# Kernel tuning notes

Measured on AMD Instinct MI355X. Metric: run time of the kernel, lower is better.

Reference implementation:

```python
import jax, jax.numpy as jnp
import numpy as np

EPS = 1e-5

def conv2d(x, w, b, pad):
    # x: [B,C,H,W], w: [O,I,kh,kw] (OIHW), b: [O]
    y = jax.lax.conv_general_dilated(x, w, (1, 1), [(pad, pad), (pad, pad)],
                                     dimension_numbers=('NCHW', 'OIHW', 'NCHW'))
    return y + b[None, :, None, None]

def bn(x, g, b, m, v):
    # eval-mode BatchNorm2d
    scale = (g / jnp.sqrt(v + EPS))[None, :, None, None]
    return (x - m[None, :, None, None]) * scale + b[None, :, None, None]


def setup_inputs() -> dict:
    key = jax.random.key(0)
    ks = jax.random.split(key, 16)
    B, C, H, W = 2, 64, 64, 64
    Cq = C // 8
    f = lambda k, shp, s=0.05: jax.random.normal(k, shp, dtype=jnp.float32) * s
    return {
        'x': jax.random.normal(ks[0], (B, C, H, W), dtype=jnp.float32),
        'sW': f(ks[1], (C, C, 3, 3)), 'sb': f(ks[2], (C,)),
        's_g': jnp.ones((C,), jnp.float32), 's_b': jnp.zeros((C,), jnp.float32),
        's_m': jnp.zeros((C,), jnp.float32), 's_v': jnp.ones((C,), jnp.float32),
        'cW': f(ks[3], (C, C, 3, 3)), 'cb': f(ks[4], (C,)),
        'c_g': jnp.ones((C,), jnp.float32), 'c_b': jnp.zeros((C,), jnp.float32),
        'c_m': jnp.zeros((C,), jnp.float32), 'c_v': jnp.ones((C,), jnp.float32),
        'qW': f(ks[5], (Cq, C, 1, 1)), 'qb': f(ks[6], (Cq,)),
        'kW': f(ks[7], (Cq, C, 1, 1)), 'kb': f(ks[8], (Cq,)),
        'vW': f(ks[9], (C, C, 1, 1)), 'vb': f(ks[10], (C,)),
        'oW': f(ks[11], (C, C, 1, 1)), 'ob': f(ks[12], (C,)),
        's_gamma': jnp.array([0.5], jnp.float32),
        'c_gamma': jnp.array([0.5], jnp.float32),
    }


def reference(x, sW, sb, s_g, s_b, s_m, s_v, cW, cb, c_g, c_b, c_m, c_v,
              qW, qb, kW, kb, vW, vb, oW, ob, s_gamma, c_gamma):
    # ---- spatial attention branch ----
    s_x = jax.nn.relu(bn(conv2d(x, sW, sb, 1), s_g, s_b, s_m, s_v))  # [B,C,H,W]
    B, C, H, W = s_x.shape
    HW = H * W
    q = conv2d(x, qW, qb, 0).reshape(B, -1, HW)  # [B, C/8, HW]
    k = conv2d(x, kW, kb, 0).reshape(B, -1, HW)  # [B, C/8, HW]
    v = conv2d(x, vW, vb, 0).reshape(B, C, HW)   # [B, C,   HW]
    # aff[b,i,j] = q_i . k_j ; softmax over j (unscaled, per original)
    A = jax.nn.softmax(jnp.einsum('bdi,bdj->bij', q, k), axis=-1)  # [B,HW,HW]
    sa = jnp.einsum('bcj,bij->bci', v, A).reshape(B, C, H, W)
    sa_map = s_gamma[0] * sa + s_x
    # ---- channel attention branch ----
    c_x = jax.nn.relu(bn(conv2d(x, cW, cb, 1), c_g, c_b, c_m, c_v))  # [B,C,H,W]
    fmap = c_x.reshape(B, C, HW)
    Ac = jnp.einsum('bin,bjn->bij', fmap, fmap)  # [B,C,C]
    Ac = jax.nn.softmax(jnp.max(Ac, axis=-1, keepdims=True) - Ac, axis=-1)
    ca = jnp.einsum('bij,bjn->bin', Ac, fmap).reshape(B, C, H, W)
    ca_map = c_gamma[0] * ca + c_x
    # ---- fuse + output adaptor ----
    return conv2d(sa_map + ca_map, oW, ob, 0)
```

## Files before the change

### kernel.cpp

```cpp
#include <hip/hip_runtime.h>

#define HW 4096

typedef __attribute__((ext_vector_type(8)))  short short8;
typedef __attribute__((ext_vector_type(16))) float float16;

__device__ __forceinline__ unsigned short f2bf(float f) {
    unsigned u = __float_as_uint(f);
    u += 0x7fffu + ((u >> 16) & 1u);
    return (unsigned short)(u >> 16);
}

__global__ __launch_bounds__(256) void k_wprep(
    const float* __restrict__ sW, const float* __restrict__ cW,
    const float* __restrict__ sb, const float* __restrict__ cb,
    const float* __restrict__ s_g, const float* __restrict__ s_b,
    const float* __restrict__ s_m, const float* __restrict__ s_v,
    const float* __restrict__ c_g, const float* __restrict__ c_b,
    const float* __restrict__ c_m, const float* __restrict__ c_v,
    unsigned short* __restrict__ Wa, float* __restrict__ scsh)
{
    int bx = blockIdx.x;
    int which = bx / 9, khw = bx % 9;
    const float* W = which ? cW : sW;
    int t = threadIdx.x;
#pragma unroll
    for (int i = 0; i < 16; i++) {
        int idx = t + 256 * i;
        int oc = idx >> 6, ic = idx & 63;
        float v = W[(size_t)(oc * 64 + ic) * 9 + khw];
        Wa[((size_t)(which * 9 + khw) * 64 + oc) * 64 + ic] = f2bf(v);
    }
    if (bx == 0 && t < 128) {
        int wh = t >> 6, oc = t & 63;
        const float* g  = wh ? c_g : s_g;
        const float* bb = wh ? c_b : s_b;
        const float* m  = wh ? c_m : s_m;
        const float* vv = wh ? c_v : s_v;
        const float* cbias = wh ? cb : sb;
        float scale = g[oc] * rsqrtf(vv[oc] + 1e-5f);
        scsh[wh * 128 + oc]      = scale;
        scsh[wh * 128 + 64 + oc] = (cbias[oc] - m[oc]) * scale + bb[oc];
    }
}

__global__ __launch_bounds__(256) void k_conv_qkv(
    const float* __restrict__ x, const unsigned short* __restrict__ Wa,
    const float* __restrict__ scsh,
    const float* __restrict__ qW, const float* __restrict__ qb,
    const float* __restrict__ kW, const float* __restrict__ kb,
    const float* __restrict__ vW, const float* __restrict__ vb,
    float* __restrict__ sx, float* __restrict__ cx,
    unsigned short* __restrict__ qT, unsigned short* __restrict__ kT,
    unsigned short* __restrict__ vB)
{
    __shared__ unsigned short xs[3 * 8 * 66 * 8];
    int bx = blockIdx.x;
    int t = threadIdx.x;

    if (bx < 256) {
        int which = bx >> 7;
        int b     = (bx >> 6) & 1;
        int row   = bx & 63;

        const float* xb = x + (size_t)(b * 64) * HW;
#pragma unroll
        for (int it = 0; it < 24; it++) {
            int idx = t + 256 * it;
            int lr  = idx >> 11;
            int rem = idx & 2047;
            int icp = rem >> 6;
            int col = rem & 63;
            int ir  = row - 1 + lr;
            unsigned pack = 0;
            if (ir >= 0 && ir < 64) {
                float v0 = xb[(size_t)(icp * 2)     * HW + ir * 64 + col];
                float v1 = xb[(size_t)(icp * 2 + 1) * HW + ir * 64 + col];
                pack = (unsigned)f2bf(v0) | ((unsigned)f2bf(v1) << 16);
            }
            int icg = icp >> 2, io = icp & 3;
            *(unsigned*)&xs[(((lr * 8 + icg) * 66 + col + 1) * 8) + io * 2] = pack;
        }
        if (t < 192) {
            int pair = t & 3;
            int colsel = (t >> 2) & 1;
            int rg = t >> 3;
            *(unsigned*)&xs[((rg * 66 + colsel * 65) * 8) + pair * 2] = 0u;
        }
        __syncthreads();

        int lane = t & 63, w = t >> 6;
        int l31 = lane & 31, half = lane >> 5;
        int colh = w & 1;
        int m0   = (w >> 1) * 32;
        int c    = colh * 32 + l31;

        float16 acc;
#pragma unroll
        for (int i = 0; i < 16; i++) acc[i] = 0.f;

        const unsigned short* Wbase =
            Wa + ((size_t)which * 9) * 4096 + (size_t)(m0 + l31) * 64 + half * 8;

#pragma unroll
        for (int khw = 0; khw < 9; khw++) {
            const int kh = khw / 3, kw = khw % 3;
#pragma unroll
            for (int icq = 0; icq < 4; icq++) {
                short8 af = *(const short8*)(Wbase + (size_t)khw * 4096 + icq * 16);
                const unsigned short* bp =
                    &xs[((kh * 8 + icq * 2 + half) * 66 + kw) * 8];
                short8 bf = *(const short8*)(bp + (size_t)c * 8);
                acc = __builtin_amdgcn_mfma_f32_32x32x16_bf16(af, bf, acc, 0, 0, 0);
            }
        }

        float* out = (which ? cx : sx) + (size_t)(b * 64) * HW;
        const float* sc = scsh + which * 128;
        int hwbase = row * 64 + c;
#pragma unroll
        for (int r = 0; r < 16; r++) {
            int oc = m0 + (r & 3) + 8 * (r >> 2) + 4 * half;
            float s  = sc[oc];
            float sh = sc[64 + oc];
            out[(size_t)oc * HW + hwbase] = fmaxf(acc[r] * s + sh, 0.f);
        }
    } else {
        int qbx = bx - 256;
        int b = qbx / 80, rem = qbx % 80;
        int chunk = rem / 5, g = rem % 5;
        int hw = chunk * 256 + t;
        const float* xb = x + (size_t)(b * 64) * HW + hw;

        float acc[16];
#pragma unroll
        for (int u = 0; u < 16; u++) acc[u] = 0.f;

        if (g == 0) {
            for (int ic = 0; ic < 64; ic++) {
                float xv = xb[ic * HW];
#pragma unroll
                for (int u = 0; u < 8; u++) acc[u]     += qW[u * 64 + ic] * xv;
#pragma unroll
                for (int u = 0; u < 8; u++) acc[8 + u] += kW[u * 64 + ic] * xv;
            }
            short8 qv, kv;
#pragma unroll
            for (int u = 0; u < 8; u++) qv[u] = (short)f2bf(acc[u] + qb[u]);
#pragma unroll
            for (int u = 0; u < 8; u++) kv[u] = (short)f2bf(acc[8 + u] + kb[u]);
            *(short8*)(qT + ((size_t)(b * HW) + hw) * 8) = qv;
            *(short8*)(kT + ((size_t)(b * HW) + hw) * 8) = kv;
        } else {
            int c0 = (g - 1) * 16;
            for (int ic = 0; ic < 64; ic++) {
                float xv = xb[ic * HW];
#pragma unroll
                for (int u = 0; u < 16; u++) acc[u] += vW[(c0 + u) * 64 + ic] * xv;
            }
            int m  = hw & 15;
            int sg = (m & 3) | ((m & 4) << 1) | ((m & 8) >> 1);
            size_t base = ((size_t)(b * 256) + (hw >> 4)) * 1024 + sg;
#pragma unroll
            for (int u = 0; u < 16; u++)
                vB[base + (size_t)(c0 + u) * 16] = f2bf(acc[u] + vb[c0 + u]);
        }
    }
}

union SmemKB {
    struct { float o_sh[4][64][33]; float den_sh[4][32]; } a;
    float slab[32][68];
};

__global__ __launch_bounds__(256) void k_attn_gram(
    const unsigned short* __restrict__ qT, const unsigned short* __restrict__ kT,
    const unsigned short* __restrict__ vB, const float* __restrict__ cx,
    float* __restrict__ Opart, float* __restrict__ denp,
    float* __restrict__ Gpart)
{
    __shared__ SmemKB sm;
    int bx = blockIdx.x;
    int t = threadIdx.x;

    if (bx < 512) {
        int lane = t & 63, w = t >> 6;
        int half = lane >> 5, l31 = lane & 31;
        int b  = bx >> 8;
        int itile = (bx >> 1) & 127;
        int jh = bx & 1;
        int i0 = itile * 32;

        short8 qf;
        if (half == 0) {
            qf = *(const short8*)(qT + ((size_t)(b * HW) + i0 + l31) * 8);
        } else {
#pragma unroll
            for (int i = 0; i < 8; i++) qf[i] = 0;
        }

        float16 o0, o1;
#pragma unroll
        for (int i = 0; i < 16; i++) { o0[i] = 0.f; o1[i] = 0.f; }
        float denr = 0.f;

        const unsigned short* kTb = kT + (size_t)(b * HW) * 8;
        const unsigned short* vBb = vB + (size_t)b * (256 * 1024);

        for (int tile = 0; tile < 16; tile++) {
            int j0 = jh * 2048 + w * 512 + tile * 32;
            int g0 = j0 >> 4;

            short8 kf;
            if (half == 0) {
                kf = *(const short8*)(kTb + (size_t)(j0 + l31) * 8);
            } else {
#pragma unroll
                for (int i = 0; i < 8; i++) kf[i] = 0;
            }

            float16 z;
#pragma unroll
            for (int i = 0; i < 16; i++) z[i] = 0.f;
            float16 s = __builtin_amdgcn_mfma_f32_32x32x16_bf16(kf, qf, z, 0, 0, 0);

            float p[16];
#pragma unroll
            for (int r = 0; r < 16; r++) {
                p[r] = __expf(s[r]);
                denr += p[r];
            }
            short8 pa0, pa1;
#pragma unroll
            for (int r = 0; r < 8; r++) {
                pa0[r] = (short)f2bf(p[r]);
                pa1[r] = (short)f2bf(p[8 + r]);
            }

            const unsigned short* vg0 = vBb + (size_t)g0 * 1024 + half * 8;
            short8 v00 = *(const short8*)(vg0 + (size_t)l31 * 16);
            short8 v01 = *(const short8*)(vg0 + (size_t)(32 + l31) * 16);
            short8 v10 = *(const short8*)(vg0 + 1024 + (size_t)l31 * 16);
            short8 v11 = *(const short8*)(vg0 + 1024 + (size_t)(32 + l31) * 16);

            o0 = __builtin_amdgcn_mfma_f32_32x32x16_bf16(pa0, v00, o0, 0, 0, 0);
            o1 = __builtin_amdgcn_mfma_f32_32x32x16_bf16(pa0, v01, o1, 0, 0, 0);
            o0 = __builtin_amdgcn_mfma_f32_32x32x16_bf16(pa1, v10, o0, 0, 0, 0);
            o1 = __builtin_amdgcn_mfma_f32_32x32x16_bf16(pa1, v11, o1, 0, 0, 0);
        }

        float dfull = denr + __shfl_xor(denr, 32);
        if (half == 0) sm.a.den_sh[w][l31] = dfull;
#pragma unroll
        for (int r = 0; r < 16; r++) {
            int il = (r & 3) + 8 * (r >> 2) + 4 * half;
            sm.a.o_sh[w][l31][il]      = o0[r];
            sm.a.o_sh[w][32 + l31][il] = o1[r];
        }
        __syncthreads();

        int i  = t & 31;
        int cg = t >> 5;
        if (cg == 0)
            denp[jh * 8192 + b * 4096 + i0 + i] =
                sm.a.den_sh[0][i] + sm.a.den_sh[1][i] +
                sm.a.den_sh[2][i] + sm.a.den_sh[3][i];
#pragma unroll
        for (int u = 0; u < 8; u++) {
            int c = cg * 8 + u;
            float sv = sm.a.o_sh[0][c][i] + sm.a.o_sh[1][c][i]
                     + sm.a.o_sh[2][c][i] + sm.a.o_sh[3][c][i];
            Opart[((size_t)(jh * 2 + b) * 64 + c) * HW + i0 + i] = sv;
        }
    } else {
        int gbx = bx - 512;
        int b = gbx >> 7, slice = gbx & 127;
        int hw0 = slice * 32;

#pragma unroll
        for (int it = 0; it < 2; it++) {
            int idx = t + 256 * it;
            int hw = idx & 31, c0 = (idx >> 5) * 4;
            float4 vv;
            vv.x = cx[(size_t)(b * 64 + c0 + 0) * HW + hw0 + hw];
            vv.y = cx[(size_t)(b * 64 + c0 + 1) * HW + hw0 + hw];
            vv.z = cx[(size_t)(b * 64 + c0 + 2) * HW + hw0 + hw];
            vv.w = cx[(size_t)(b * 64 + c0 + 3) * HW + hw0 + hw];
            *(float4*)&sm.slab[hw][c0] = vv;
        }
        __syncthreads();

        int i0 = (t & 15) * 4, j0 = (t >> 4) * 4;
        float acc[4][4] = {};
#pragma unroll 8
        for (int hw = 0; hw < 32; hw++) {
            float4 ai = *(const float4*)&sm.slab[hw][i0];
            float4 aj = *(const float4*)&sm.slab[hw][j0];
            acc[0][0] += ai.x * aj.x; acc[0][1] += ai.x * aj.y;
            acc[0][2] += ai.x * aj.z; acc[0][3] += ai.x * aj.w;
            acc[1][0] += ai.y * aj.x; acc[1][1] += ai.y * aj.y;
            acc[1][2] += ai.y * aj.z; acc[1][3] += ai.y * aj.w;
            acc[2][0] += ai.z * aj.x; acc[2][1] += ai.z * aj.y;
            acc[2][2] += ai.z * aj.z; acc[2][3] += ai.z * aj.w;
            acc[3][0] += ai.w * aj.x; acc[3][1] += ai.w * aj.y;
            acc[3][2] += ai.w * aj.z; acc[3][3] += ai.w * aj.w;
        }

        float* Gb = Gpart + ((size_t)(b * 128 + slice) * 64) * 64;
#pragma unroll
        for (int ii = 0; ii < 4; ii++)
            *(float4*)&Gb[(size_t)(i0 + ii) * 64 + j0] =
                make_float4(acc[ii][0], acc[ii][1], acc[ii][2], acc[ii][3]);
    }
}

__global__ __launch_bounds__(64) void k_csoft(
    const float* __restrict__ Gpart, float* __restrict__ AcsT)
{
    int row = blockIdx.x;
    int b = row >> 6, i = row & 63;
    int j = threadIdx.x;

    const float* Gp = Gpart + ((size_t)(b * 128) * 64 + i) * 64 + j;
    float a = 0.f;
#pragma unroll 4
    for (int sl = 0; sl < 128; sl++)
        a += Gp[(size_t)sl * 4096];

    float mn = a;
    mn = fminf(mn, __shfl_xor(mn, 1));
    mn = fminf(mn, __shfl_xor(mn, 2));
    mn = fminf(mn, __shfl_xor(mn, 4));
    mn = fminf(mn, __shfl_xor(mn, 8));
    mn = fminf(mn, __shfl_xor(mn, 16));
    mn = fminf(mn, __shfl_xor(mn, 32));
    float p = __expf(mn - a);
    float s = p;
    s += __shfl_xor(s, 1);
    s += __shfl_xor(s, 2);
    s += __shfl_xor(s, 4);
    s += __shfl_xor(s, 8);
    s += __shfl_xor(s, 16);
    s += __shfl_xor(s, 32);
    AcsT[(size_t)b * 4096 + j * 64 + i] = p / s;
}

__global__ __launch_bounds__(256) void k_fuse_out(
    const float* __restrict__ Opart, const float* __restrict__ denp,
    const float* __restrict__ sx,    const float* __restrict__ cx,
    const float* __restrict__ AcsT,
    const float* __restrict__ oW,    const float* __restrict__ ob,
    const float* __restrict__ s_gamma, const float* __restrict__ c_gamma,
    float* __restrict__ out)
{
    __shared__ float A_sh[64][68];
    __shared__ float cxs[64][33];
    __shared__ float f_sh[64][33];
    __shared__ float oWT[64][68];

    int bx = blockIdx.x;
    int b = bx >> 7, chunk = bx & 127;
    int px0 = chunk * 32;
    int t = threadIdx.x;
    float sgam = s_gamma[0], cgam = c_gamma[0];

#pragma unroll
    for (int k = 0; k < 16; k++) {
        int idx = t + 256 * k;
        int j = idx >> 6, i = idx & 63;
        A_sh[j][i] = AcsT[(size_t)b * 4096 + idx];
        oWT[j][i]  = oW[(size_t)i * 64 + j];
    }
#pragma unroll
    for (int k = 0; k < 8; k++) {
        int idx = t + 256 * k;
        int c = idx >> 5, px = idx & 31;
        size_t o = (size_t)(b * 64 + c) * HW + px0 + px;
        float cv = cx[o];
        cxs[c][px] = cv;
        float d = denp[b * 4096 + px0 + px] + denp[8192 + b * 4096 + px0 + px];
        float O = Opart[((size_t)(b)*64 + c) * HW + px0 + px]
                + Opart[((size_t)(2 + b) * 64 + c) * HW + px0 + px];
        f_sh[c][px] = sgam * (O / d) + sx[o] + cv;
    }
    __syncthreads();

    {
        int px = t & 31, cg = t >> 5;
        int c0 = cg * 8;
        float ca[8] = {};
        for (int j = 0; j < 64; j++) {
            float xv = cxs[j][px];
            float4 a0 = *(const float4*)&A_sh[j][c0];
            float4 a1 = *(const float4*)&A_sh[j][c0 + 4];
            ca[0] += a0.x * xv; ca[1] += a0.y * xv;
            ca[2] += a0.z * xv; ca[3] += a0.w * xv;
            ca[4] += a1.x * xv; ca[5] += a1.y * xv;
            ca[6] += a1.z * xv; ca[7] += a1.w * xv;
        }
#pragma unroll
        for (int u = 0; u < 8; u++)
            f_sh[c0 + u][px] += cgam * ca[u];
    }
    __syncthreads();

    {
        int px = t & 31, og = t >> 5;
        int o0 = og * 8;
        float acc[8] = {};
        for (int c = 0; c < 64; c++) {
            float fv = f_sh[c][px];
            float4 a0 = *(const float4*)&oWT[c][o0];
            float4 a1 = *(const float4*)&oWT[c][o0 + 4];
            acc[0] += a0.x * fv; acc[1] += a0.y * fv;
            acc[2] += a0.z * fv; acc[3] += a0.w * fv;
            acc[4] += a1.x * fv; acc[5] += a1.y * fv;
            acc[6] += a1.z * fv; acc[7] += a1.w * fv;
        }
#pragma unroll
        for (int u = 0; u < 8; u++) {
            int o = o0 + u;
            out[(size_t)(b * 64 + o) * HW + px0 + px] = acc[u] + ob[o];
        }
    }
}

extern "C" void kernel_launch(void* const* d_in, const int* in_sizes, int n_in,
                              void* d_out, int out_size, void* d_ws, size_t ws_size,
                              hipStream_t stream)
{
    const float* x    = (const float*)d_in[0];
    const float* sW   = (const float*)d_in[1];
    const float* sb   = (const float*)d_in[2];
    const float* s_g  = (const float*)d_in[3];
    const float* s_b  = (const float*)d_in[4];
    const float* s_m  = (const float*)d_in[5];
    const float* s_v  = (const float*)d_in[6];
    const float* cW   = (const float*)d_in[7];
    const float* cb   = (const float*)d_in[8];
    const float* c_g  = (const float*)d_in[9];
    const float* c_b  = (const float*)d_in[10];
    const float* c_m  = (const float*)d_in[11];
    const float* c_v  = (const float*)d_in[12];
    const float* qW   = (const float*)d_in[13];
    const float* qb   = (const float*)d_in[14];
    const float* kW   = (const float*)d_in[15];
    const float* kb   = (const float*)d_in[16];
    const float* vW   = (const float*)d_in[17];
    const float* vb   = (const float*)d_in[18];
    const float* oW   = (const float*)d_in[19];
    const float* ob   = (const float*)d_in[20];
    const float* s_gamma = (const float*)d_in[21];
    const float* c_gamma = (const float*)d_in[22];

    float* ws    = (float*)d_ws;
    float* sx    = ws;
    float* cx    = ws + 524288;
    float* Opart = ws + 1048576;
    float* denp  = ws + 2097152;
    float* AcsT  = ws + 2113536;
    float* Gpart = ws + 2121728;
    float* scsh  = ws + 3170304;
    unsigned short* us = (unsigned short*)(ws + 3170560);
    unsigned short* qT = us;
    unsigned short* kT = us + 65536;
    unsigned short* vB = us + 131072;
    unsigned short* Wa = us + 655360;

    k_wprep<<<18, 256, 0, stream>>>(sW, cW, sb, cb, s_g, s_b, s_m, s_v,
                                    c_g, c_b, c_m, c_v, Wa, scsh);
    k_conv_qkv<<<416, 256, 0, stream>>>(x, Wa, scsh, qW, qb, kW, kb, vW, vb,
                                        sx, cx, qT, kT, vB);
    k_attn_gram<<<768, 256, 0, stream>>>(qT, kT, vB, cx, Opart, denp, Gpart);
    k_csoft<<<128, 64, 0, stream>>>(Gpart, AcsT);
    k_fuse_out<<<256, 256, 0, stream>>>(Opart, denp, sx, cx, AcsT,
                                        oW, ob, s_gamma, c_gamma, (float*)d_out);
}
```

Baseline: 170.9 us.

## Fuse all stages into one persistent kernel with grid-wide barriers

Merges the five separate launches (weight prep, conv/QKV, attention+Gram, channel softmax, fuse/output) into a single 512-block kernel separated by atomic-counter grid barriers. It also reshapes work along the way: fewer, larger Gram slices, and a single-block channel softmax per batch. The oW transpose moves into the prep stage, and the output stage uses 16-pixel chunks across all 512 blocks. The goal is to remove inter-kernel launch gaps and tail idle time. In exchange it relies on all 512 blocks being co-resident and on a barrier reset trick that assumes the counter cell holds a 0xAA fill pattern before each call.

```diff
diff --git a/kernel.cpp b/kernel.cpp
--- a/kernel.cpp
+++ b/kernel.cpp
@@ -1,6 +1,7 @@
 #include <hip/hip_runtime.h>
 
 #define HW 4096
+#define NBLK 512
 
 typedef __attribute__((ext_vector_type(8)))  short short8;
 typedef __attribute__((ext_vector_type(16))) float float16;
@@ -11,59 +12,87 @@
     return (unsigned short)(u >> 16);
 }
 
-__global__ __launch_bounds__(256) void k_wprep(
-    const float* __restrict__ sW, const float* __restrict__ cW,
-    const float* __restrict__ sb, const float* __restrict__ cb,
-    const float* __restrict__ s_g, const float* __restrict__ s_b,
-    const float* __restrict__ s_m, const float* __restrict__ s_v,
-    const float* __restrict__ c_g, const float* __restrict__ c_b,
-    const float* __restrict__ c_m, const float* __restrict__ c_v,
-    unsigned short* __restrict__ Wa, float* __restrict__ scsh)
+struct Params {
+    const float *x;
+    const float *sW, *sb, *s_g, *s_b, *s_m, *s_v;
+    const float *cW, *cb, *c_g, *c_b, *c_m, *c_v;
+    const float *qW, *qb, *kW, *kb, *vW, *vb, *oW, *ob;
+    const float *s_gamma, *c_gamma;
+    float *out;
+    float *sx, *cx, *Opart, *denp, *ATg, *Gpart, *oWTg, *scsh;
+    unsigned *bar;
+    unsigned short *qT, *kT, *vB, *Wa;
+};
+
+union SmemAll {
+    unsigned short xs[3 * 8 * 66 * 8];
+    struct { float o_sh[4][64][33]; float den_sh[4][32]; } at;
+    float slab[64][68];
+    struct {
+        float AT[64][68];
+        union {
+            float A_raw[64][68];
+            struct { float cxs[64][17]; float f_sh[64][17];
+                     float oWT[64][68]; } f;
+        } u;
+    } d;
+};
+
+__device__ __forceinline__ void gridbar(unsigned* cell)
 {
+    __syncthreads();
+    if (threadIdx.x == 0) {
+        __threadfence();
+        atomicCAS(cell, 0xAAAAAAAAu, 0u);
+        atomicAdd(cell, 1u);
+        while (atomicAdd(cell, 0u) < NBLK) __builtin_amdgcn_s_sleep(8);
+        __threadfence();
+    }
+    __syncthreads();
+}
+
+__global__ __launch_bounds__(256, 2) void k_mega(Params p)
+{
+    __shared__ SmemAll sm;
     int bx = blockIdx.x;
-    int which = bx / 9, khw = bx % 9;
-    const float* W = which ? cW : sW;
-    int t = threadIdx.x;
-#pragma unroll
-    for (int i = 0; i < 16; i++) {
-        int idx = t + 256 * i;
-        int oc = idx >> 6, ic = idx & 63;
-        float v = W[(size_t)(oc * 64 + ic) * 9 + khw];
-        Wa[((size_t)(which * 9 + khw) * 64 + oc) * 64 + ic] = f2bf(v);
-    }
-    if (bx == 0 && t < 128) {
-        int wh = t >> 6, oc = t & 63;
-        const float* g  = wh ? c_g : s_g;
-        const float* bb = wh ? c_b : s_b;
-        const float* m  = wh ? c_m : s_m;
-        const float* vv = wh ? c_v : s_v;
-        const float* cbias = wh ? cb : sb;
-        float scale = g[oc] * rsqrtf(vv[oc] + 1e-5f);
-        scsh[wh * 128 + oc]      = scale;
-        scsh[wh * 128 + 64 + oc] = (cbias[oc] - m[oc]) * scale + bb[oc];
-    }
-}
-
-__global__ __launch_bounds__(256) void k_conv_qkv(
-    const float* __restrict__ x, const unsigned short* __restrict__ Wa,
-    const float* __restrict__ scsh,
-    const float* __restrict__ qW, const float* __restrict__ qb,
-    const float* __restrict__ kW, const float* __restrict__ kb,
-    const float* __restrict__ vW, const float* __restrict__ vb,
-    float* __restrict__ sx, float* __restrict__ cx,
-    unsigned short* __restrict__ qT, unsigned short* __restrict__ kT,
-    unsigned short* __restrict__ vB)
-{
-    __shared__ unsigned short xs[3 * 8 * 66 * 8];
-    int bx = blockIdx.x;
-    int t = threadIdx.x;
+    int t  = threadIdx.x;
+
+    if (bx < 18) {
+        int which = bx / 9, khw = bx % 9;
+        const float* W = which ? p.cW : p.sW;
+#pragma unroll
+        for (int i = 0; i < 16; i++) {
+            int idx = t + 256 * i;
+            int oc = idx >> 6, ic = idx & 63;
+            float v = W[(size_t)(oc * 64 + ic) * 9 + khw];
+            p.Wa[((size_t)(which * 9 + khw) * 64 + oc) * 64 + ic] = f2bf(v);
+        }
+        if (bx == 0 && t < 128) {
+            int wh = t >> 6, oc = t & 63;
+            const float* g  = wh ? p.c_g : p.s_g;
+            const float* bb = wh ? p.c_b : p.s_b;
+            const float* m  = wh ? p.c_m : p.s_m;
+            const float* vv = wh ? p.c_v : p.s_v;
+            const float* cbias = wh ? p.cb : p.sb;
+            float scale = g[oc] * rsqrtf(vv[oc] + 1e-5f);
+            p.scsh[wh * 128 + oc]      = scale;
+            p.scsh[wh * 128 + 64 + oc] = (cbias[oc] - m[oc]) * scale + bb[oc];
+        }
+    } else if (bx == 18) {
+#pragma unroll
+        for (int k = 0; k < 16; k++) {
+            int idx = t + 256 * k;
+            int c = idx >> 6, o = idx & 63;
+            p.oWTg[idx] = p.oW[(size_t)o * 64 + c];
+        }
+    }
+    gridbar(p.bar + 0);
 
     if (bx < 256) {
         int which = bx >> 7;
         int b     = (bx >> 6) & 1;
         int row   = bx & 63;
-
-        const float* xb = x + (size_t)(b * 64) * HW;
+        const float* xb = p.x + (size_t)(b * 64) * HW;
 #pragma unroll
         for (int it = 0; it < 24; it++) {
             int idx = t + 256 * it;
@@ -79,13 +108,13 @@
                 pack = (unsigned)f2bf(v0) | ((unsigned)f2bf(v1) << 16);
             }
             int icg = icp >> 2, io = icp & 3;
-            *(unsigned*)&xs[(((lr * 8 + icg) * 66 + col + 1) * 8) + io * 2] = pack;
+            *(unsigned*)&sm.xs[(((lr * 8 + icg) * 66 + col + 1) * 8) + io * 2] = pack;
         }
         if (t < 192) {
             int pair = t & 3;
             int colsel = (t >> 2) & 1;
             int rg = t >> 3;
-            *(unsigned*)&xs[((rg * 66 + colsel * 65) * 8) + pair * 2] = 0u;
+            *(unsigned*)&sm.xs[((rg * 66 + colsel * 65) * 8) + pair * 2] = 0u;
         }
         __syncthreads();
 
@@ -100,7 +129,7 @@
         for (int i = 0; i < 16; i++) acc[i] = 0.f;
 
         const unsigned short* Wbase =
-            Wa + ((size_t)which * 9) * 4096 + (size_t)(m0 + l31) * 64 + half * 8;
+            p.Wa + ((size_t)which * 9) * 4096 + (size_t)(m0 + l31) * 64 + half * 8;
 
 #pragma unroll
         for (int khw = 0; khw < 9; khw++) {
@@ -109,14 +138,14 @@
             for (int icq = 0; icq < 4; icq++) {
                 short8 af = *(const short8*)(Wbase + (size_t)khw * 4096 + icq * 16);
                 const unsigned short* bp =
-                    &xs[((kh * 8 + icq * 2 + half) * 66 + kw) * 8];
+                    &sm.xs[((kh * 8 + icq * 2 + half) * 66 + kw) * 8];
                 short8 bf = *(const short8*)(bp + (size_t)c * 8);
                 acc = __builtin_amdgcn_mfma_f32_32x32x16_bf16(af, bf, acc, 0, 0, 0);
             }
         }
 
-        float* out = (which ? cx : sx) + (size_t)(b * 64) * HW;
-        const float* sc = scsh + which * 128;
+        float* out = (which ? p.cx : p.sx) + (size_t)(b * 64) * HW;
+        const float* sc = p.scsh + which * 128;
         int hwbase = row * 64 + c;
 #pragma unroll
         for (int r = 0; r < 16; r++) {
@@ -125,12 +154,12 @@
             float sh = sc[64 + oc];
             out[(size_t)oc * HW + hwbase] = fmaxf(acc[r] * s + sh, 0.f);
         }
-    } else {
-        int qbx = bx - 256;
-        int b = qbx / 80, rem = qbx % 80;
+    } else if (bx < 416) {
+        int ubx = bx - 256;
+        int b = ubx / 80, rem = ubx % 80;
         int chunk = rem / 5, g = rem % 5;
         int hw = chunk * 256 + t;
-        const float* xb = x + (size_t)(b * 64) * HW + hw;
+        const float* xb = p.x + (size_t)(b * 64) * HW + hw;
 
         float acc[16];
 #pragma unroll
@@ -140,50 +169,35 @@
             for (int ic = 0; ic < 64; ic++) {
                 float xv = xb[ic * HW];
 #pragma unroll
-                for (int u = 0; u < 8; u++) acc[u]     += qW[u * 64 + ic] * xv;
-#pragma unroll
-                for (int u = 0; u < 8; u++) acc[8 + u] += kW[u * 64 + ic] * xv;
+                for (int u = 0; u < 8; u++) acc[u]     += p.qW[u * 64 + ic] * xv;
+#pragma unroll
+                for (int u = 0; u < 8; u++) acc[8 + u] += p.kW[u * 64 + ic] * xv;
             }
             short8 qv, kv;
 #pragma unroll
-            for (int u = 0; u < 8; u++) qv[u] = (short)f2bf(acc[u] + qb[u]);
-#pragma unroll
-            for (int u = 0; u < 8; u++) kv[u] = (short)f2bf(acc[8 + u] + kb[u]);
-            *(short8*)(qT + ((size_t)(b * HW) + hw) * 8) = qv;
-            *(short8*)(kT + ((size_t)(b * HW) + hw) * 8) = kv;
+            for (int u = 0; u < 8; u++) qv[u] = (short)f2bf(acc[u] + p.qb[u]);
+#pragma unroll
+            for (int u = 0; u < 8; u++) kv[u] = (short)f2bf(acc[8 + u] + p.kb[u]);
+            *(short8*)(p.qT + ((size_t)(b * HW) + hw) * 8) = qv;
+            *(short8*)(p.kT + ((size_t)(b * HW) + hw) * 8) = kv;
         } else {
             int c0 = (g - 1) * 16;
             for (int ic = 0; ic < 64; ic++) {
                 float xv = xb[ic * HW];
 #pragma unroll
-                for (int u = 0; u < 16; u++) acc[u] += vW[(c0 + u) * 64 + ic] * xv;
+                for (int u = 0; u < 16; u++) acc[u] += p.vW[(c0 + u) * 64 + ic] * xv;
             }
             int m  = hw & 15;
             int sg = (m & 3) | ((m & 4) << 1) | ((m & 8) >> 1);
             size_t base = ((size_t)(b * 256) + (hw >> 4)) * 1024 + sg;
 #pragma unroll
             for (int u = 0; u < 16; u++)
-                vB[base + (size_t)(c0 + u) * 16] = f2bf(acc[u] + vb[c0 + u]);
-        }
-    }
-}
-
-union SmemKB {
-    struct { float o_sh[4][64][33]; float den_sh[4][32]; } a;
-    float slab[32][68];
-};
-
-__global__ __launch_bounds__(256) void k_attn_gram(
-    const unsigned short* __restrict__ qT, const unsigned short* __restrict__ kT,
-    const unsigned short* __restrict__ vB, const float* __restrict__ cx,
-    float* __restrict__ Opart, float* __restrict__ denp,
-    float* __restrict__ Gpart)
-{
-    __shared__ SmemKB sm;
-    int bx = blockIdx.x;
-    int t = threadIdx.x;
-
-    if (bx < 512) {
+                p.vB[base + (size_t)(c0 + u) * 16] = f2bf(acc[u] + p.vb[c0 + u]);
+        }
+    }
+    gridbar(p.bar + 1);
+
+    {
         int lane = t & 63, w = t >> 6;
         int half = lane >> 5, l31 = lane & 31;
         int b  = bx >> 8;
@@ -193,7 +207,7 @@
 
         short8 qf;
         if (half == 0) {
-            qf = *(const short8*)(qT + ((size_t)(b * HW) + i0 + l31) * 8);
+            qf = *(const short8*)(p.qT + ((size_t)(b * HW) + i0 + l31) * 8);
         } else {
 #pragma unroll
             for (int i = 0; i < 8; i++) qf[i] = 0;
@@ -204,8 +218,8 @@
         for (int i = 0; i < 16; i++) { o0[i] = 0.f; o1[i] = 0.f; }
         float denr = 0.f;
 
-        const unsigned short* kTb = kT + (size_t)(b * HW) * 8;
-        const unsigned short* vBb = vB + (size_t)b * (256 * 1024);
+        const unsigned short* kTb = p.kT + (size_t)(b * HW) * 8;
+        const unsigned short* vBb = p.vB + (size_t)b * (256 * 1024);
 
         for (int tile = 0; tile < 16; tile++) {
             int j0 = jh * 2048 + w * 512 + tile * 32;
@@ -224,17 +238,17 @@
             for (int i = 0; i < 16; i++) z[i] = 0.f;
             float16 s = __builtin_amdgcn_mfma_f32_32x32x16_bf16(kf, qf, z, 0, 0, 0);
 
-            float p[16];
+            float pr[16];
 #pragma unroll
             for (int r = 0; r < 16; r++) {
-                p[r] = __expf(s[r]);
-                denr += p[r];
+                pr[r] = __expf(s[r]);
+                denr += pr[r];
             }
             short8 pa0, pa1;
 #pragma unroll
             for (int r = 0; r < 8; r++) {
-                pa0[r] = (short)f2bf(p[r]);
-                pa1[r] = (short)f2bf(p[8 + r]);
+                pa0[r] = (short)f2bf(pr[r]);
+                pa1[r] = (short)f2bf(pr[8 + r]);
             }
 
             const unsigned short* vg0 = vBb + (size_t)g0 * 1024 + half * 8;
@@ -250,177 +264,154 @@
         }
 
         float dfull = denr + __shfl_xor(denr, 32);
-        if (half == 0) sm.a.den_sh[w][l31] = dfull;
+        if (half == 0) sm.at.den_sh[w][l31] = dfull;
 #pragma unroll
         for (int r = 0; r < 16; r++) {
             int il = (r & 3) + 8 * (r >> 2) + 4 * half;
-            sm.a.o_sh[w][l31][il]      = o0[r];
-            sm.a.o_sh[w][32 + l31][il] = o1[r];
+            sm.at.o_sh[w][l31][il]      = o0[r];
+            sm.at.o_sh[w][32 + l31][il] = o1[r];
         }
         __syncthreads();
 
         int i  = t & 31;
         int cg = t >> 5;
         if (cg == 0)
-            denp[jh * 8192 + b * 4096 + i0 + i] =
-                sm.a.den_sh[0][i] + sm.a.den_sh[1][i] +
-                sm.a.den_sh[2][i] + sm.a.den_sh[3][i];
+            p.denp[jh * 8192 + b * 4096 + i0 + i] =
+                sm.at.den_sh[0][i] + sm.at.den_sh[1][i] +
+                sm.at.den_sh[2][i] + sm.at.den_sh[3][i];
 #pragma unroll
         for (int u = 0; u < 8; u++) {
             int c = cg * 8 + u;
-            float sv = sm.a.o_sh[0][c][i] + sm.a.o_sh[1][c][i]
-                     + sm.a.o_sh[2][c][i] + sm.a.o_sh[3][c][i];
-            Opart[((size_t)(jh * 2 + b) * 64 + c) * HW + i0 + i] = sv;
-        }
-    } else {
-        int gbx = bx - 512;
-        int b = gbx >> 7, slice = gbx & 127;
-        int hw0 = slice * 32;
-
-#pragma unroll
-        for (int it = 0; it < 2; it++) {
-            int idx = t + 256 * it;
-            int hw = idx & 31, c0 = (idx >> 5) * 4;
-            float4 vv;
-            vv.x = cx[(size_t)(b * 64 + c0 + 0) * HW + hw0 + hw];
-            vv.y = cx[(size_t)(b * 64 + c0 + 1) * HW + hw0 + hw];
-            vv.z = cx[(size_t)(b * 64 + c0 + 2) * HW + hw0 + hw];
-            vv.w = cx[(size_t)(b * 64 + c0 + 3) * HW + hw0 + hw];
-            *(float4*)&sm.slab[hw][c0] = vv;
+            float sv = sm.at.o_sh[0][c][i] + sm.at.o_sh[1][c][i]
+                     + sm.at.o_sh[2][c][i] + sm.at.o_sh[3][c][i];
+            p.Opart[((size_t)(jh * 2 + b) * 64 + c) * HW + i0 + i] = sv;
+        }
+    }
+    if (bx >= 448) {
+        int gbx = bx - 448;
+        int b = gbx >> 5, slice = gbx & 31;
+        int i0 = (t & 15) * 4, j0c = (t >> 4) * 4;
+        float acc[4][4] = {};
+#pragma unroll
+        for (int ch = 0; ch < 2; ch++) {
+            int hwb = slice * 128 + ch * 64;
+            __syncthreads();
+#pragma unroll
+            for (int it = 0; it < 16; it++) {
+                int idx = t + 256 * it;
+                int hw = idx & 63, c = idx >> 6;
+                sm.slab[hw][c] = p.cx[(size_t)(b * 64 + c) * HW + hwb + hw];
+            }
+            __syncthreads();
+#pragma unroll 8
+            for (int hw = 0; hw < 64; hw++) {
+                float4 ai = *(const float4*)&sm.slab[hw][i0];
+                float4 aj = *(const float4*)&sm.slab[hw][j0c];
+                acc[0][0] += ai.x * aj.x; acc[0][1] += ai.x * aj.y;
+                acc[0][2] += ai.x * aj.z; acc[0][3] += ai.x * aj.w;
+                acc[1][0] += ai.y * aj.x; acc[1][1] += ai.y * aj.y;
+                acc[1][2] += ai.y * aj.z; acc[1][3] += ai.y * aj.w;
+                acc[2][0] += ai.z * aj.x; acc[2][1] += ai.z * aj.y;
+                acc[2][2] += ai.z * aj.z; acc[2][3] += ai.z * aj.w;
+                acc[3][0] += ai.w * aj.x; acc[3][1] += ai.w * aj.y;
+                acc[3][2] += ai.w * aj.z; acc[3][3] += ai.w * aj.w;
+            }
+        }
+        float* Gb = p.Gpart + ((size_t)(b * 32 + slice)) * 4096;
+#pragma unroll
+        for (int ii = 0; ii < 4; ii++)
+            *(float4*)&Gb[(size_t)(i0 + ii) * 64 + j0c] =
+                make_float4(acc[ii][0], acc[ii][1], acc[ii][2], acc[ii][3]);
+    }
+    gridbar(p.bar + 2);
+
+    if (bx < 2) {
+        int b = bx;
+#pragma unroll
+        for (int k = 0; k < 16; k++) {
+            int idx = t + 256 * k;
+            float a = 0.f;
+#pragma unroll 8
+            for (int sl = 0; sl < 32; sl++)
+                a += p.Gpart[((size_t)(b * 32 + sl)) * 4096 + idx];
+            sm.d.u.A_raw[idx >> 6][idx & 63] = a;
         }
         __syncthreads();
-
-        int i0 = (t & 15) * 4, j0 = (t >> 4) * 4;
-        float acc[4][4] = {};
+        if (t < 64) {
+            int i = t;
+            float mn = sm.d.u.A_raw[i][0];
 #pragma unroll 8
-        for (int hw = 0; hw < 32; hw++) {
-            float4 ai = *(const float4*)&sm.slab[hw][i0];
-            float4 aj = *(const float4*)&sm.slab[hw][j0];
-            acc[0][0] += ai.x * aj.x; acc[0][1] += ai.x * aj.y;
-            acc[0][2] += ai.x * aj.z; acc[0][3] += ai.x * aj.w;
-            acc[1][0] += ai.y * aj.x; acc[1][1] += ai.y * aj.y;
-            acc[1][2] += ai.y * aj.z; acc[1][3] += ai.y * aj.w;
-            acc[2][0] += ai.z * aj.x; acc[2][1] += ai.z * aj.y;
-            acc[2][2] += ai.z * aj.z; acc[2][3] += ai.z * aj.w;
-            acc[3][0] += ai.w * aj.x; acc[3][1] += ai.w * aj.y;
-            acc[3][2] += ai.w * aj.z; acc[3][3] += ai.w * aj.w;
-        }
-
-        float* Gb = Gpart + ((size_t)(b * 128 + slice) * 64) * 64;
-#pragma unroll
-        for (int ii = 0; ii < 4; ii++)
-            *(float4*)&Gb[(size_t)(i0 + ii) * 64 + j0] =
-                make_float4(acc[ii][0], acc[ii][1], acc[ii][2], acc[ii][3]);
-    }
-}
-
-__global__ __launch_bounds__(64) void k_csoft(
-    const float* __restrict__ Gpart, float* __restrict__ AcsT)
-{
-    int row = blockIdx.x;
-    int b = row >> 6, i = row & 63;
-    int j = threadIdx.x;
-
-    const float* Gp = Gpart + ((size_t)(b * 128) * 64 + i) * 64 + j;
-    float a = 0.f;
-#pragma unroll 4
-    for (int sl = 0; sl < 128; sl++)
-        a += Gp[(size_t)sl * 4096];
-
-    float mn = a;
-    mn = fminf(mn, __shfl_xor(mn, 1));
-    mn = fminf(mn, __shfl_xor(mn, 2));
-    mn = fminf(mn, __shfl_xor(mn, 4));
-    mn = fminf(mn, __shfl_xor(mn, 8));
-    mn = fminf(mn, __shfl_xor(mn, 16));
-    mn = fminf(mn, __shfl_xor(mn, 32));
-    float p = __expf(mn - a);
-    float s = p;
-    s += __shfl_xor(s, 1);
-    s += __shfl_xor(s, 2);
-    s += __shfl_xor(s, 4);
-    s += __shfl_xor(s, 8);
-    s += __shfl_xor(s, 16);
-    s += __shfl_xor(s, 32);
-    AcsT[(size_t)b * 4096 + j * 64 + i] = p / s;
-}
-
-__global__ __launch_bounds__(256) void k_fuse_out(
-    const float* __restrict__ Opart, const float* __restrict__ denp,
-    const float* __restrict__ sx,    const float* __restrict__ cx,
-    const float* __restrict__ AcsT,
-    const float* __restrict__ oW,    const float* __restrict__ ob,
-    const float* __restrict__ s_gamma, const float* __restrict__ c_gamma,
-    float* __restrict__ out)
-{
-    __shared__ float A_sh[64][68];
-    __shared__ float cxs[64][33];
-    __shared__ float f_sh[64][33];
-    __shared__ float oWT[64][68];
-
-    int bx = blockIdx.x;
-    int b = bx >> 7, chunk = bx & 127;
-    int px0 = chunk * 32;
-    int t = threadIdx.x;
-    float sgam = s_gamma[0], cgam = c_gamma[0];
-
-#pragma unroll
-    for (int k = 0; k < 16; k++) {
-        int idx = t + 256 * k;
-        int j = idx >> 6, i = idx & 63;
-        A_sh[j][i] = AcsT[(size_t)b * 4096 + idx];
-        oWT[j][i]  = oW[(size_t)i * 64 + j];
-    }
-#pragma unroll
-    for (int k = 0; k < 8; k++) {
-        int idx = t + 256 * k;
-        int c = idx >> 5, px = idx & 31;
-        size_t o = (size_t)(b * 64 + c) * HW + px0 + px;
-        float cv = cx[o];
-        cxs[c][px] = cv;
-        float d = denp[b * 4096 + px0 + px] + denp[8192 + b * 4096 + px0 + px];
-        float O = Opart[((size_t)(b)*64 + c) * HW + px0 + px]
-                + Opart[((size_t)(2 + b) * 64 + c) * HW + px0 + px];
-        f_sh[c][px] = sgam * (O / d) + sx[o] + cv;
-    }
-    __syncthreads();
+            for (int j = 1; j < 64; j++) mn = fminf(mn, sm.d.u.A_raw[i][j]);
+            float ssum = 0.f;
+#pragma unroll 8
+            for (int j = 0; j < 64; j++) ssum += __expf(mn - sm.d.u.A_raw[i][j]);
+            float inv = 1.f / ssum;
+#pragma unroll 8
+            for (int j = 0; j < 64; j++)
+                p.ATg[(size_t)b * 4096 + j * 64 + i] =
+                    __expf(mn - sm.d.u.A_raw[i][j]) * inv;
+        }
+    }
+    gridbar(p.bar + 3);
 
     {
-        int px = t & 31, cg = t >> 5;
-        int c0 = cg * 8;
-        float ca[8] = {};
-        for (int j = 0; j < 64; j++) {
-            float xv = cxs[j][px];
-            float4 a0 = *(const float4*)&A_sh[j][c0];
-            float4 a1 = *(const float4*)&A_sh[j][c0 + 4];
-            ca[0] += a0.x * xv; ca[1] += a0.y * xv;
-            ca[2] += a0.z * xv; ca[3] += a0.w * xv;
-            ca[4] += a1.x * xv; ca[5] += a1.y * xv;
-            ca[6] += a1.z * xv; ca[7] += a1.w * xv;
-        }
-#pragma unroll
-        for (int u = 0; u < 8; u++)
-            f_sh[c0 + u][px] += cgam * ca[u];
-    }
-    __syncthreads();
-
-    {
-        int px = t & 31, og = t >> 5;
-        int o0 = og * 8;
-        float acc[8] = {};
-        for (int c = 0; c < 64; c++) {
-            float fv = f_sh[c][px];
-            float4 a0 = *(const float4*)&oWT[c][o0];
-            float4 a1 = *(const float4*)&oWT[c][o0 + 4];
-            acc[0] += a0.x * fv; acc[1] += a0.y * fv;
-            acc[2] += a0.z * fv; acc[3] += a0.w * fv;
-            acc[4] += a1.x * fv; acc[5] += a1.y * fv;
-            acc[6] += a1.z * fv; acc[7] += a1.w * fv;
-        }
-#pragma unroll
-        for (int u = 0; u < 8; u++) {
-            int o = o0 + u;
-            out[(size_t)(b * 64 + o) * HW + px0 + px] = acc[u] + ob[o];
+        int b = bx >> 8, chunk = bx & 255;
+        int px0 = chunk * 16;
+        float sgam = p.s_gamma[0], cgam = p.c_gamma[0];
+
+#pragma unroll
+        for (int k = 0; k < 16; k++) {
+            int idx = t + 256 * k;
+            int j = idx >> 6, i = idx & 63;
+            sm.d.AT[j][i]      = p.ATg[(size_t)b * 4096 + idx];
+            sm.d.u.f.oWT[j][i] = p.oWTg[idx];
+        }
+#pragma unroll
+        for (int k = 0; k < 4; k++) {
+            int idx = t + 256 * k;
+            int c = idx >> 4, px = idx & 15;
+            size_t o = (size_t)(b * 64 + c) * HW + px0 + px;
+            float cv = p.cx[o];
+            sm.d.u.f.cxs[c][px] = cv;
+            float dd = p.denp[b * 4096 + px0 + px]
+                     + p.denp[8192 + b * 4096 + px0 + px];
+            float O = p.Opart[((size_t)(b) * 64 + c) * HW + px0 + px]
+                    + p.Opart[((size_t)(2 + b) * 64 + c) * HW + px0 + px];
+            sm.d.u.f.f_sh[c][px] = sgam * (O / dd) + p.sx[o] + cv;
+        }
+        __syncthreads();
+
+        {
+            int px = t & 15, cg = t >> 4;
+            int c0 = cg * 4;
+            float ca[4] = {};
+            for (int j = 0; j < 64; j++) {
+                float xv = sm.d.u.f.cxs[j][px];
+                float4 a = *(const float4*)&sm.d.AT[j][c0];
+                ca[0] += a.x * xv; ca[1] += a.y * xv;
+                ca[2] += a.z * xv; ca[3] += a.w * xv;
+            }
+#pragma unroll
+            for (int u = 0; u < 4; u++)
+                sm.d.u.f.f_sh[c0 + u][px] += cgam * ca[u];
+        }
+        __syncthreads();
+
+        {
+            int px = t & 15, og = t >> 4;
+            int o0 = og * 4;
+            float acc[4] = {};
+            for (int c = 0; c < 64; c++) {
+                float fv = sm.d.u.f.f_sh[c][px];
+                float4 wv = *(const float4*)&sm.d.u.f.oWT[c][o0];
+                acc[0] += wv.x * fv; acc[1] += wv.y * fv;
+                acc[2] += wv.z * fv; acc[3] += wv.w * fv;
+            }
+#pragma unroll
+            for (int u = 0; u < 4; u++) {
+                int o = o0 + u;
+                p.out[(size_t)(b * 64 + o) * HW + px0 + px] = acc[u] + p.ob[o];
+            }
         }
     }
 }
@@ -429,50 +420,38 @@
                               void* d_out, int out_size, void* d_ws, size_t ws_size,
                               hipStream_t stream)
 {
-    const float* x    = (const float*)d_in[0];
-    const float* sW   = (const float*)d_in[1];
-    const float* sb   = (const float*)d_in[2];
-    const float* s_g  = (const float*)d_in[3];
-    const float* s_b  = (const float*)d_in[4];
-    const float* s_m  = (const float*)d_in[5];
-    const float* s_v  = (const float*)d_in[6];
-    const float* cW   = (const float*)d_in[7];
-    const float* cb   = (const float*)d_in[8];
-    const float* c_g  = (const float*)d_in[9];
-    const float* c_b  = (const float*)d_in[10];
-    const float* c_m  = (const float*)d_in[11];
-    const float* c_v  = (const float*)d_in[12];
-    const float* qW   = (const float*)d_in[13];
-    const float* qb   = (const float*)d_in[14];
-    const float* kW   = (const float*)d_in[15];
-    const float* kb   = (const float*)d_in[16];
-    const float* vW   = (const float*)d_in[17];
-    const float* vb   = (const float*)d_in[18];
-    const float* oW   = (const float*)d_in[19];
-    const float* ob   = (const float*)d_in[20];
-    const float* s_gamma = (const float*)d_in[21];
-    const float* c_gamma = (const float*)d_in[22];
-
-    float* ws    = (float*)d_ws;
-    float* sx    = ws;
-    float* cx    = ws + 524288;
-    float* Opart = ws + 1048576;
-    float* denp  = ws + 2097152;
-    float* AcsT  = ws + 2113536;
-    float* Gpart = ws + 2121728;
-    float* scsh  = ws + 3170304;
-    unsigned short* us = (unsigned short*)(ws + 3170560);
-    unsigned short* qT = us;
-    unsigned short* kT = us + 65536;
-    unsigned short* vB = us + 131072;
-    unsigned short* Wa = us + 655360;
-
-    k_wprep<<<18, 256, 0, stream>>>(sW, cW, sb, cb, s_g, s_b, s_m, s_v,
-                                    c_g, c_b, c_m, c_v, Wa, scsh);
-    k_conv_qkv<<<416, 256, 0, stream>>>(x, Wa, scsh, qW, qb, kW, kb, vW, vb,
-                                        sx, cx, qT, kT, vB);
-    k_attn_gram<<<768, 256, 0, stream>>>(qT, kT, vB, cx, Opart, denp, Gpart);
-    k_csoft<<<128, 64, 0, stream>>>(Gpart, AcsT);
-    k_fuse_out<<<256, 256, 0, stream>>>(Opart, denp, sx, cx, AcsT,
-                                        oW, ob, s_gamma, c_gamma, (float*)d_out);
+    float* ws = (float*)d_ws;
+
+    Params P;
+    P.x  = (const float*)d_in[0];
+    P.sW = (const float*)d_in[1];  P.sb = (const float*)d_in[2];
+    P.s_g = (const float*)d_in[3]; P.s_b = (const float*)d_in[4];
+    P.s_m = (const float*)d_in[5]; P.s_v = (const float*)d_in[6];
+    P.cW = (const float*)d_in[7];  P.cb = (const float*)d_in[8];
+    P.c_g = (const float*)d_in[9]; P.c_b = (const float*)d_in[10];
+    P.c_m = (const float*)d_in[11]; P.c_v = (const float*)d_in[12];
+    P.qW = (const float*)d_in[13]; P.qb = (const float*)d_in[14];
+    P.kW = (const float*)d_in[15]; P.kb = (const float*)d_in[16];
+    P.vW = (const float*)d_in[17]; P.vb = (const float*)d_in[18];
+    P.oW = (const float*)d_in[19]; P.ob = (const float*)d_in[20];
+    P.s_gamma = (const float*)d_in[21];
+    P.c_gamma = (const float*)d_in[22];
+    P.out = (float*)d_out;
+
+    P.sx    = ws;
+    P.cx    = ws + 524288;
+    P.Opart = ws + 1048576;
+    P.denp  = ws + 2097152;
+    P.ATg   = ws + 2113536;
+    P.Gpart = ws + 2121728;
+    P.oWTg  = ws + 2383872;
+    P.scsh  = ws + 2387968;
+    P.bar   = (unsigned*)(ws + 2388224);
+    unsigned short* us = (unsigned short*)(ws + 2388240);
+    P.qT = us;
+    P.kT = us + 65536;
+    P.vB = us + 131072;
+    P.Wa = us + 655360;
+
+    k_mega<<<NBLK, 256, 0, stream>>>(P);
 }
```

Result: slower. 375.0 us (+119.4%).
